# Optimization experiments

Measured on AMD Instinct MI355X. Metric: run time of the kernel, lower is better.

Reference implementation:

```python
import jax, jax.numpy as jnp
import numpy as np

EPS = 1e-08


def setup_inputs() -> dict:
    key = jax.random.key(0)
    k1, k2 = jax.random.split(key)
    n, d = 8192, 64
    x = jax.random.normal(k1, (n, d), dtype=jnp.float32)
    y = jax.random.randint(k2, (n,), 0, 10, dtype=jnp.int64)
    # weights = 1 / temperature_init = 1 / 0.1
    weights = jnp.full((1,), 10.0, dtype=jnp.float32)
    return {"x": x, "y": y, "weights": weights}


def reference(x, y, weights):
    n = x.shape[0]
    # pairwise euclidean distances (torch.cdist p=2)
    sq = jnp.sum(x * x, axis=1)                      # [n]
    d2 = sq[:, None] + sq[None, :] - 2.0 * (x @ x.T)  # [n,n]
    eye = jnp.eye(n, dtype=bool)
    d2 = jnp.maximum(d2, 0.0)
    dist = jnp.where(eye, 0.0, jnp.sqrt(jnp.where(eye, 1.0, d2)))  # safe sqrt on diag
    expo = jnp.exp(-dist * weights[0])               # [n,n]
    same = (y[:, None] == y[None, :]) & ~eye         # same-class, excluding self
    top = jnp.sum(jnp.where(same, expo, 0.0), axis=1)  # [n]
    bot = jnp.sum(jnp.where(~eye, expo, 0.0), axis=1)  # [n]
    fracs = jnp.log(top / (bot + EPS))
    loss = -jnp.mean(fracs)
    return loss
```

## Files before the change

kernel.cpp:

```cpp
#include <hip/hip_runtime.h>

typedef _Float16 f16x8 __attribute__((ext_vector_type(8)));
typedef float    f32x4 __attribute__((ext_vector_type(4)));

#define N_ROWS 8192
#define DIM 64
#define EPS 1e-8f
#define LOG2E 1.4426950408889634f
#define SHIFT 64.0f
#define SHIFT_LN 44.361419555836499802f
#define TILE_I 256
#define NBI (N_ROWS / TILE_I)
#define TB 512
#define MAXC 17


__global__ void snn_prep(const float* __restrict__ x, _Float16* __restrict__ xh,
                         _Float16* __restrict__ xl, float* __restrict__ sq,
                         float* __restrict__ top, float* __restrict__ bot,
                         float* __restrict__ out) {
    const int gt = blockIdx.x * 256 + threadIdx.x;
    if (gt < N_ROWS) { top[gt] = 0.0f; bot[gt] = 0.0f; }
    if (gt == 0) out[0] = 0.0f;
    const int row = gt >> 6, lane = threadIdx.x & 63;
    float v = x[row * DIM + lane];
    _Float16 h = (_Float16)v;
    _Float16 l = (_Float16)(v - (float)h);
    xh[row * DIM + lane] = h;
    xl[row * DIM + lane] = l;
    float s = v * v;
    #pragma unroll
    for (int off = 32; off > 0; off >>= 1) s += __shfl_xor(s, off, 64);
    if (lane == 0) sq[row] = s;
}

__global__ __launch_bounds__(256, 2) void snn_mfma(
    const _Float16* __restrict__ xh, const _Float16* __restrict__ xl,
    const float* __restrict__ sq, const int* __restrict__ y,
    const float* __restrict__ w,
    float* __restrict__ top, float* __restrict__ bot)
{
    __shared__ float s_sqj[MAXC * 16];
    __shared__ int   s_yj[MAXC * 16];
    __shared__ float s_jt[4][MAXC * 16];
    __shared__ float s_jb[4][MAXC * 16];

    const int bid = blockIdx.x;
    int bi = 0, kk = 0, cum = 0;
    for (int p = 0; p < NBI; p++) {
        int nb = (p < 16) ? p + 1 : p;
        if (bid < cum + nb) { bi = p; kk = bid - cum; break; }
        cum += nb;
    }
    int c0, len;
    if (bi < 16)      { c0 = 16 * kk;              len = 16; }
    else if (kk < 16) { c0 = 17 * kk;              len = 17; }
    else              { c0 = 272 + 16 * (kk - 16); len = 16; }
    const int ndch = min(max(16 * bi - c0, 0), len);
    const int I0 = bi * TILE_I;

    const int tid = threadIdx.x, wv = tid >> 6, lane = tid & 63;
    const int mrow = lane & 15, kq = lane >> 4;

    for (int t = tid; t < len * 16; t += 256) {
        s_sqj[t] = sq[c0 * 16 + t];
        s_yj[t]  = y[c0 * 16 + t];
    }
    __syncthreads();

    const int iw = I0 + wv * 64;

    f16x8 ah[4][2], al[4][2];
    #pragma unroll
    for (int mt = 0; mt < 4; mt++)
        #pragma unroll
        for (int kc = 0; kc < 2; kc++) {
            int a = (iw + mt * 16 + mrow) * DIM + kc * 32 + kq * 8;
            ah[mt][kc] = *(const f16x8*)(xh + a);
            al[mt][kc] = *(const f16x8*)(xl + a);
        }

    float sqi[4][4]; int ypack[4];
    #pragma unroll
    for (int mt = 0; mt < 4; mt++) {
        int yp = 0;
        #pragma unroll
        for (int rr = 0; rr < 4; rr++) {
            int i = iw + mt * 16 + kq * 4 + rr;
            sqi[mt][rr] = sq[i];
            yp |= (y[i] & 255) << (8 * rr);
        }
        ypack[mt] = yp;
    }

    float ts[4][4], bs[4][4];
    #pragma unroll
    for (int mt = 0; mt < 4; mt++)
        #pragma unroll
        for (int rr = 0; rr < 4; rr++) { ts[mt][rr] = 0.0f; bs[mt][rr] = 0.0f; }

    const float c1 = -w[0] * LOG2E;
    f32x4 acc[4];

#define DECL_LOAD(N, NTL)                                                        \
    const int jr##N = (c0 + (NTL)) * 16 + mrow;                                  \
    const int boff##N = jr##N * DIM + kq * 8;                                    \
    f16x8 cbh0##N = *(const f16x8*)(xh + boff##N);                               \
    f16x8 cbh1##N = *(const f16x8*)(xh + boff##N + 32);                          \
    f16x8 cbl0##N = *(const f16x8*)(xl + boff##N);                               \
    f16x8 cbl1##N = *(const f16x8*)(xl + boff##N + 32);                          \
    const float sqj##N = s_sqj[(NTL) * 16 + mrow];                               \
    const int   yj##N  = s_yj[(NTL) * 16 + mrow];

#define DO_MFMA(N)                                                               \
    _Pragma("unroll")                                                            \
    for (int mt = 0; mt < 4; mt++) acc[mt] = (f32x4){0.f, 0.f, 0.f, 0.f};        \
    _Pragma("unroll")                                                            \
    for (int mt = 0; mt < 4; mt++)                                               \
        acc[mt] = __builtin_amdgcn_mfma_f32_16x16x32_f16(ah[mt][0], cbh0##N, acc[mt], 0, 0, 0); \
    _Pragma("unroll")                                                            \
    for (int mt = 0; mt < 4; mt++)                                               \
        acc[mt] = __builtin_amdgcn_mfma_f32_16x16x32_f16(ah[mt][1], cbh1##N, acc[mt], 0, 0, 0); \
    _Pragma("unroll")                                                            \
    for (int mt = 0; mt < 4; mt++)                                               \
        acc[mt] = __builtin_amdgcn_mfma_f32_16x16x32_f16(ah[mt][0], cbl0##N, acc[mt], 0, 0, 0); \
    _Pragma("unroll")                                                            \
    for (int mt = 0; mt < 4; mt++)                                               \
        acc[mt] = __builtin_amdgcn_mfma_f32_16x16x32_f16(ah[mt][1], cbl1##N, acc[mt], 0, 0, 0); \
    _Pragma("unroll")                                                            \
    for (int mt = 0; mt < 4; mt++)                                               \
        acc[mt] = __builtin_amdgcn_mfma_f32_16x16x32_f16(al[mt][0], cbh0##N, acc[mt], 0, 0, 0); \
    _Pragma("unroll")                                                            \
    for (int mt = 0; mt < 4; mt++)                                               \
        acc[mt] = __builtin_amdgcn_mfma_f32_16x16x32_f16(al[mt][1], cbh1##N, acc[mt], 0, 0, 0);

#define EPI_BOTH(N, NTL)                                                         \
    {                                                                            \
        float jt = 0.0f, jb = 0.0f;                                              \
        _Pragma("unroll")                                                        \
        for (int mt = 0; mt < 4; mt++)                                           \
            _Pragma("unroll")                                                    \
            for (int rr = 0; rr < 4; rr++) {                                     \
                float d2 = fmaf(-2.0f, acc[mt][rr], sqi[mt][rr] + sqj##N);       \
                d2 = fmaxf(d2, 0.0f);                                            \
                float dist = __builtin_amdgcn_sqrtf(d2);                         \
                float e2 = __builtin_amdgcn_exp2f(fmaf(c1, dist, SHIFT));        \
                float e2t = (yj##N == ((ypack[mt] >> (8 * rr)) & 255)) ? e2 : 0.0f; \
                ts[mt][rr] += e2t;                                               \
                bs[mt][rr] += e2;                                                \
                jt += e2t;                                                       \
                jb += e2;                                                        \
            }                                                                    \
        jt += __shfl_xor(jt, 16, 64); jt += __shfl_xor(jt, 32, 64);              \
        jb += __shfl_xor(jb, 16, 64); jb += __shfl_xor(jb, 32, 64);              \
        if (kq == 0) {                                                           \
            s_jt[wv][(NTL) * 16 + mrow] = jt;                                    \
            s_jb[wv][(NTL) * 16 + mrow] = jb;                                    \
        }                                                                        \
    }

#define EPI_DIAG(N, NTL)                                                         \
    {                                                                            \
        _Pragma("unroll")                                                        \
        for (int mt = 0; mt < 4; mt++)                                           \
            _Pragma("unroll")                                                    \
            for (int rr = 0; rr < 4; rr++) {                                     \
                int i = iw + mt * 16 + kq * 4 + rr;                              \
                float d2 = fmaf(-2.0f, acc[mt][rr], sqi[mt][rr] + sqj##N);       \
                d2 = fmaxf(d2, 0.0f);                                            \
                float dist = __builtin_amdgcn_sqrtf(d2);                         \
                float e2 = __builtin_amdgcn_exp2f(fmaf(c1, dist, SHIFT));        \
                bool offd = (i != jr##N);                                        \
                bool same = offd && (yj##N == ((ypack[mt] >> (8 * rr)) & 255));  \
                bs[mt][rr] += offd ? e2 : 0.0f;                                  \
                ts[mt][rr] += same ? e2 : 0.0f;                                  \
            }                                                                    \
    }

    int ntl = 0;
    for (; ntl + 2 <= ndch; ntl += 2) {
        DECL_LOAD(0, ntl)
        DECL_LOAD(1, ntl + 1)
        DO_MFMA(0)
        EPI_BOTH(0, ntl)
        DO_MFMA(1)
        EPI_BOTH(1, ntl + 1)
    }
    for (; ntl < ndch; ntl++) {
        DECL_LOAD(0, ntl)
        DO_MFMA(0)
        EPI_BOTH(0, ntl)
    }
    for (; ntl + 2 <= len; ntl += 2) {
        DECL_LOAD(0, ntl)
        DECL_LOAD(1, ntl + 1)
        DO_MFMA(0)
        EPI_DIAG(0, ntl)
        DO_MFMA(1)
        EPI_DIAG(1, ntl + 1)
    }
    for (; ntl < len; ntl++) {
        DECL_LOAD(0, ntl)
        DO_MFMA(0)
        EPI_DIAG(0, ntl)
    }
#undef DECL_LOAD
#undef DO_MFMA
#undef EPI_BOTH
#undef EPI_DIAG

    #pragma unroll
    for (int mt = 0; mt < 4; mt++)
        #pragma unroll
        for (int rr = 0; rr < 4; rr++) {
            float tv = ts[mt][rr], bv = bs[mt][rr];
            #pragma unroll
            for (int off = 1; off < 16; off <<= 1) {
                tv += __shfl_xor(tv, off, 64);
                bv += __shfl_xor(bv, off, 64);
            }
            if (mrow == 0) {
                int i = iw + mt * 16 + kq * 4 + rr;
                atomicAdd(&top[i], tv);
                atomicAdd(&bot[i], bv);
            }
        }

    if (ndch > 0) {
        __syncthreads();
        for (int t = tid; t < ndch * 16; t += 256) {
            float tt = s_jt[0][t] + s_jt[1][t] + s_jt[2][t] + s_jt[3][t];
            float bb = s_jb[0][t] + s_jb[1][t] + s_jb[2][t] + s_jb[3][t];
            atomicAdd(&top[c0 * 16 + t], tt);
            atomicAdd(&bot[c0 * 16 + t], bb);
        }
    }
}

__global__ __launch_bounds__(256) void snn_final(
    const float* __restrict__ top, const float* __restrict__ bot,
    float* __restrict__ out)
{
    const int i = blockIdx.x * 256 + threadIdx.x;
    float t = top[i];
    float b = bot[i] * 0x1p-64f + EPS;
    float acc = (logf(t) - SHIFT_LN) - logf(b);
    #pragma unroll
    for (int off = 32; off > 0; off >>= 1) acc += __shfl_xor(acc, off, 64);
    __shared__ float red[4];
    if ((threadIdx.x & 63) == 0) red[threadIdx.x >> 6] = acc;
    __syncthreads();
    if (threadIdx.x == 0) {
        float s = red[0] + red[1] + red[2] + red[3];
        atomicAdd(out, -s / (float)N_ROWS);
    }
}

extern "C" void kernel_launch(void* const* d_in, const int* in_sizes, int n_in,
                              void* d_out, int out_size, void* d_ws, size_t ws_size,
                              hipStream_t stream) {
    const float* x = (const float*)d_in[0];
    const int*   y = (const int*)d_in[1];
    const float* w = (const float*)d_in[2];
    float* out = (float*)d_out;

    float* ws  = (float*)d_ws;
    float* top = ws;
    float* bot = ws + N_ROWS;
    float* sq  = ws + 2 * N_ROWS;
    _Float16* xh = (_Float16*)(ws + 3 * N_ROWS);
    _Float16* xl = xh + (size_t)N_ROWS * DIM;

    snn_prep<<<N_ROWS / 4, 256, 0, stream>>>(x, xh, xl, sq, top, bot, out);
    snn_mfma<<<TB, 256, 0, stream>>>(xh, xl, sq, y, w, top, bot);
    snn_final<<<N_ROWS / 256, 256, 0, stream>>>(top, bot, out);
}
```

Before: 94.73 us.

## Unroll column tiles by four and defer column-sum shuffles to shared memory

```diff
diff --git a/kernel.cpp b/kernel.cpp
--- a/kernel.cpp
+++ b/kernel.cpp
@@ -42,8 +42,8 @@
 {
     __shared__ float s_sqj[MAXC * 16];
     __shared__ int   s_yj[MAXC * 16];
-    __shared__ float s_jt[4][MAXC * 16];
-    __shared__ float s_jb[4][MAXC * 16];
+    __shared__ float s_jt[4][4][MAXC * 16];
+    __shared__ float s_jb[4][4][MAXC * 16];
 
     const int bid = blockIdx.x;
     int bi = 0, kk = 0, cum = 0;
@@ -151,12 +151,8 @@
                 jt += e2t;                                                       \
                 jb += e2;                                                        \
             }                                                                    \
-        jt += __shfl_xor(jt, 16, 64); jt += __shfl_xor(jt, 32, 64);              \
-        jb += __shfl_xor(jb, 16, 64); jb += __shfl_xor(jb, 32, 64);              \
-        if (kq == 0) {                                                           \
-            s_jt[wv][(NTL) * 16 + mrow] = jt;                                    \
-            s_jb[wv][(NTL) * 16 + mrow] = jb;                                    \
-        }                                                                        \
+        s_jt[wv][kq][(NTL) * 16 + mrow] = jt;     \
+        s_jb[wv][kq][(NTL) * 16 + mrow] = jb;                                    \
     }
 
 #define EPI_DIAG(N, NTL)                                                         \
@@ -178,31 +174,45 @@
     }
 
     int ntl = 0;
+    for (; ntl + 4 <= ndch; ntl += 4) {
+        DECL_LOAD(0, ntl)
+        DECL_LOAD(1, ntl + 1)
+        DECL_LOAD(2, ntl + 2)
+        DECL_LOAD(3, ntl + 3)
+        DO_MFMA(0) EPI_BOTH(0, ntl)
+        DO_MFMA(1) EPI_BOTH(1, ntl + 1)
+        DO_MFMA(2) EPI_BOTH(2, ntl + 2)
+        DO_MFMA(3) EPI_BOTH(3, ntl + 3)
+    }
     for (; ntl + 2 <= ndch; ntl += 2) {
         DECL_LOAD(0, ntl)
         DECL_LOAD(1, ntl + 1)
-        DO_MFMA(0)
-        EPI_BOTH(0, ntl)
-        DO_MFMA(1)
-        EPI_BOTH(1, ntl + 1)
+        DO_MFMA(0) EPI_BOTH(0, ntl)
+        DO_MFMA(1) EPI_BOTH(1, ntl + 1)
     }
     for (; ntl < ndch; ntl++) {
         DECL_LOAD(0, ntl)
-        DO_MFMA(0)
-        EPI_BOTH(0, ntl)
+        DO_MFMA(0) EPI_BOTH(0, ntl)
+    }
+    for (; ntl + 4 <= len; ntl += 4) {
+        DECL_LOAD(0, ntl)
+        DECL_LOAD(1, ntl + 1)
+        DECL_LOAD(2, ntl + 2)
+        DECL_LOAD(3, ntl + 3)
+        DO_MFMA(0) EPI_DIAG(0, ntl)
+        DO_MFMA(1) EPI_DIAG(1, ntl + 1)
+        DO_MFMA(2) EPI_DIAG(2, ntl + 2)
+        DO_MFMA(3) EPI_DIAG(3, ntl + 3)
     }
     for (; ntl + 2 <= len; ntl += 2) {
         DECL_LOAD(0, ntl)
         DECL_LOAD(1, ntl + 1)
-        DO_MFMA(0)
-        EPI_DIAG(0, ntl)
-        DO_MFMA(1)
-        EPI_DIAG(1, ntl + 1)
+        DO_MFMA(0) EPI_DIAG(0, ntl)
+        DO_MFMA(1) EPI_DIAG(1, ntl + 1)
     }
     for (; ntl < len; ntl++) {
         DECL_LOAD(0, ntl)
-        DO_MFMA(0)
-        EPI_DIAG(0, ntl)
+        DO_MFMA(0) EPI_DIAG(0, ntl)
     }
 #undef DECL_LOAD
 #undef DO_MFMA
@@ -229,8 +239,14 @@
     if (ndch > 0) {
         __syncthreads();
         for (int t = tid; t < ndch * 16; t += 256) {
-            float tt = s_jt[0][t] + s_jt[1][t] + s_jt[2][t] + s_jt[3][t];
-            float bb = s_jb[0][t] + s_jb[1][t] + s_jb[2][t] + s_jb[3][t];
+            float tt = 0.0f, bb = 0.0f;
+            #pragma unroll
+            for (int v = 0; v < 4; v++)
+                #pragma unroll
+                for (int q = 0; q < 4; q++) {
+                    tt += s_jt[v][q][t];
+                    bb += s_jb[v][q][t];
+                }
             atomicAdd(&top[c0 * 16 + t], tt);
             atomicAdd(&bot[c0 * 16 + t], bb);
         }
```

Result: slower. 123.9 us (+30.8%).
